# Kernel optimization log

Hardware: AMD Instinct MI355X
Metric: run time of the kernel (lower is better)

Reference implementation:

```python
import jax, jax.numpy as jnp
import numpy as np

B, S, E, H, O = 4, 2048, 1024, 8, 128

def setup_inputs() -> dict:
    key = jax.random.key(0)
    k1, k2, k3, k4, k5 = jax.random.split(key, 5)
    return {
        "x":  jax.random.normal(k1, (B, S, E), dtype=jnp.float32),
        "Wq": jax.random.normal(k2, (H, E, O), dtype=jnp.float32),
        "Wk": jax.random.normal(k3, (E, O), dtype=jnp.float32),
        "Wv": jax.random.normal(k4, (E, O), dtype=jnp.float32),
        "Wo": jax.random.normal(k5, (O * H, E), dtype=jnp.float32),
    }

def reference(x, Wq, Wk, Wv, Wo):
    # self-attention: kv = x; mode='multihead' (no causal mask), attn_mask=None
    Q = jnp.einsum('bse,heo->bhso', x, Wq)        # (B,H,S,O) per-head query proj
    K = x @ Wk                                     # (B,S,O) shared across heads
    V = x @ Wv                                     # (B,S,O)
    scale = 1.0 / jnp.sqrt(jnp.float32(O))
    scores = jnp.einsum('bhqo,bko->bhqk', Q, K) * scale  # (B,H,S,S)
    probs = jax.nn.softmax(scores, axis=-1)
    ctx = jnp.einsum('bhqk,bko->bhqo', probs, V)   # (B,H,S,O)
    ctx = ctx.transpose(0, 2, 1, 3).reshape(B, S, H * O)  # (B,S,H*O)
    return ctx @ Wo                                # (B,S,E)
```

## Files before the change

### kernel.cpp

```cpp
#include <hip/hip_runtime.h>
#include <math.h>


typedef __attribute__((ext_vector_type(8))) short bf16x8;
typedef __attribute__((ext_vector_type(4))) float f32x4;

#define MFMA(a, b, c) __builtin_amdgcn_mfma_f32_16x16x32_bf16((a), (b), (c), 0, 0, 0)
#define GLB(p) ((const __attribute__((address_space(1))) void*)(p))
#define LDS(p) ((__attribute__((address_space(3))) void*)(p))

#if __has_builtin(__builtin_amdgcn_exp2f)
#define EXP2F(x) __builtin_amdgcn_exp2f(x)
#else
#define EXP2F(x) exp2f(x)
#endif

__device__ __forceinline__ short f2bf(float f) {
    union { float f; unsigned u; } v; v.f = f;
    unsigned r = v.u + 0x7fffu + ((v.u >> 16) & 1u);
    return (short)(r >> 16);
}
__device__ __forceinline__ float bf2f(short s) {
    union { unsigned u; float f; } v; v.u = ((unsigned)(unsigned short)s) << 16;
    return v.f;
}


__global__ __launch_bounds__(256) void split_kernel(
    const float* __restrict__ x, short* __restrict__ hi, short* __restrict__ lo, int n) {
    for (int i = blockIdx.x * blockDim.x + threadIdx.x; i < n; i += gridDim.x * blockDim.x) {
        float f = x[i];
        short h = f2bf(f);
        hi[i] = h;
        lo[i] = f2bf(f - bf2f(h));
    }
}

__global__ __launch_bounds__(256) void build_wt(
    const float* __restrict__ Wq, const float* __restrict__ Wk, const float* __restrict__ Wv,
    short* __restrict__ wth, short* __restrict__ wtl) {
    const int total = 1280 * 1024;
    for (int idx = blockIdx.x * blockDim.x + threadIdx.x; idx < total; idx += gridDim.x * blockDim.x) {
        int n = idx >> 10, k = idx & 1023;
        float f;
        if (n < 1024)      f = Wq[((size_t)(n >> 7) * 1024 + k) * 128 + (n & 127)];
        else if (n < 1152) f = Wk[(size_t)k * 128 + (n - 1024)];
        else               f = Wv[(size_t)k * 128 + (n - 1152)];
        short h = f2bf(f);
        wth[idx] = h;
        wtl[idx] = f2bf(f - bf2f(h));
    }
}

__global__ __launch_bounds__(256) void build_wot(
    const float* __restrict__ Wo, short* __restrict__ wot) {
    const int total = 1024 * 1024;
    for (int idx = blockIdx.x * blockDim.x + threadIdx.x; idx < total; idx += gridDim.x * blockDim.x) {
        int e = idx >> 10, k = idx & 1023;
        wot[idx] = f2bf(Wo[(size_t)k * 1024 + e]);
    }
}

template <int MODE>
__global__ __launch_bounds__(256, 4) void gemm_k(
    const short* __restrict__ Ah, const short* __restrict__ Al,
    const short* __restrict__ Bth, const short* __restrict__ Btl,
    short* __restrict__ qh, short* __restrict__ ql,
    short* __restrict__ kh, short* __restrict__ kl,
    short* __restrict__ vt, float* __restrict__ outf) {
    constexpr int K = 1024;
    __shared__ __align__(16) char smem[33792];
    short* As_h = (short*)smem;
    short* Bs_h = (short*)(smem + 8192);
    short* As_l = (short*)(smem + 16384);
    short* Bs_l = (short*)(smem + 24576);
    unsigned* Ep = (unsigned*)smem;

    const int t = threadIdx.x;
    const int m0 = blockIdx.x * 128, n0 = blockIdx.y * 128;
    const int wave = t >> 6, lane = t & 63;
    const int wr = wave >> 1, wc = wave & 1;
    const int quad = lane >> 4, l16 = lane & 15;

    f32x4 acc[4][4];
    for (int i = 0; i < 4; ++i)
        for (int j = 0; j < 4; ++j) acc[i][j] = (f32x4){0.f, 0.f, 0.f, 0.f};

    for (int kb = 0; kb < K / 32; ++kb) {
        __syncthreads();
        for (int i = 0; i < 2; ++i) {
            int slot = (wave * 2 + i) * 64 + lane;
            int row = slot >> 2, ch = slot & 3;
            int ldsoff = (wave * 2 + i) * 512;
            size_t ga = (size_t)(m0 + row) * K + kb * 32 + ch * 8;
            size_t gb = (size_t)(n0 + row) * K + kb * 32 + ch * 8;
            __builtin_amdgcn_global_load_lds(GLB(Ah + ga), LDS(&As_h[ldsoff]), 16, 0, 0);
            __builtin_amdgcn_global_load_lds(GLB(Bth + gb), LDS(&Bs_h[ldsoff]), 16, 0, 0);
            if constexpr (MODE == 0) {
                __builtin_amdgcn_global_load_lds(GLB(Al + ga), LDS(&As_l[ldsoff]), 16, 0, 0);
                __builtin_amdgcn_global_load_lds(GLB(Btl + gb), LDS(&Bs_l[ldsoff]), 16, 0, 0);
            }
        }
        __syncthreads();

        bf16x8 a[4], b[4];
        for (int mi = 0; mi < 4; ++mi)
            a[mi] = *(const bf16x8*)&As_h[(wr * 64 + mi * 16 + l16) * 32 + quad * 8];
        for (int ni = 0; ni < 4; ++ni)
            b[ni] = *(const bf16x8*)&Bs_h[(wc * 64 + ni * 16 + l16) * 32 + quad * 8];
        for (int mi = 0; mi < 4; ++mi)
            for (int ni = 0; ni < 4; ++ni)
                acc[mi][ni] = MFMA(a[mi], b[ni], acc[mi][ni]);
        if constexpr (MODE == 0) {
            bf16x8 al[4], bl[4];
            for (int mi = 0; mi < 4; ++mi)
                al[mi] = *(const bf16x8*)&As_l[(wr * 64 + mi * 16 + l16) * 32 + quad * 8];
            for (int ni = 0; ni < 4; ++ni)
                bl[ni] = *(const bf16x8*)&Bs_l[(wc * 64 + ni * 16 + l16) * 32 + quad * 8];
            for (int mi = 0; mi < 4; ++mi)
                for (int ni = 0; ni < 4; ++ni) {
                    acc[mi][ni] = MFMA(a[mi], bl[ni], acc[mi][ni]);
                    acc[mi][ni] = MFMA(al[mi], b[ni], acc[mi][ni]);
                }
        }
    }

    const float qscale = 0.12753102455195157f;
    for (int p = 0; p < 2; ++p) {
        __syncthreads();
        if (wr == p) {
            for (int mi = 0; mi < 4; ++mi) {
                int rl = mi * 16 + quad * 4;
                for (int ni = 0; ni < 4; ++ni) {
                    int cl = wc * 64 + ni * 16 + l16;
                    for (int r = 0; r < 4; ++r) {
                        float v = acc[mi][ni][r];
                        unsigned pk;
                        if constexpr (MODE == 0) {
                            if (blockIdx.y < 8) v *= qscale;
                            short hv = f2bf(v);
                            short lv = f2bf(v - bf2f(hv));
                            pk = (unsigned)(unsigned short)hv |
                                 ((unsigned)(unsigned short)lv << 16);
                        } else {
                            union { float f; unsigned u; } cv; cv.f = v; pk = cv.u;
                        }
                        Ep[(rl + r) * 132 + cl] = pk;
                    }
                }
            }
        }
        __syncthreads();

        if constexpr (MODE == 1) {
            for (int j = 0; j < 8; ++j) {
                int cid = t + j * 256;
                int row = cid >> 5, c = cid & 31;
                f32x4 val;
                for (int q = 0; q < 4; ++q) {
                    union { unsigned u; float f; } cv;
                    cv.u = Ep[row * 132 + c * 4 + q];
                    val[q] = cv.f;
                }
                int gr = m0 + p * 64 + row;
                *(f32x4*)&outf[(size_t)gr * 1024 + n0 + c * 4] = val;
            }
        } else if (blockIdx.y < 9) {
            for (int j = 0; j < 4; ++j) {
                int cid = t + j * 256;
                int row = cid >> 4, c = cid & 15;
                bf16x8 hv, lv;
                for (int q = 0; q < 8; ++q) {
                    unsigned w = Ep[row * 132 + c * 8 + q];
                    hv[q] = (short)(w & 0xffffu);
                    lv[q] = (short)(w >> 16);
                }
                int gr = m0 + p * 64 + row;
                int bb = gr >> 11, s = gr & 2047;
                if (blockIdx.y < 8) {
                    size_t base = (((size_t)(bb * 8 + (n0 >> 7))) * 2048 + s) * 128 + c * 8;
                    *(bf16x8*)&qh[base] = hv;
                    *(bf16x8*)&ql[base] = lv;
                } else {
                    size_t base = ((size_t)bb * 2048 + s) * 128 + c * 8;
                    *(bf16x8*)&kh[base] = hv;
                    *(bf16x8*)&kl[base] = lv;
                }
            }
        } else {
            for (int j = 0; j < 4; ++j) {
                int cid = t + j * 256;
                int d = cid >> 3, sc = cid & 7;
                bf16x8 hv;
                for (int q = 0; q < 8; ++q) {
                    unsigned w = Ep[(sc * 8 + q) * 132 + d];
                    hv[q] = (short)(w & 0xffffu);
                }
                int gr0 = m0 + p * 64 + sc * 8;
                int bb = gr0 >> 11, s0 = gr0 & 2047;
                *(bf16x8*)&vt[((size_t)bb * 128 + d) * 2048 + s0] = hv;
            }
        }
    }
}

__global__ __launch_bounds__(256, 2) void attn_k(
    const short* __restrict__ qh, const short* __restrict__ ql,
    const short* __restrict__ kh, const short* __restrict__ kl,
    const short* __restrict__ vt, short* __restrict__ ctx) {
    constexpr int S = 2048, D = 128;
    __shared__ short Kh_s[64 * 128];
    __shared__ short Kl_s[64 * 128];
    __shared__ short Vt_s[128 * 64];
    __shared__ short P_s[128 * 72];

    const int bh = blockIdx.y, b = bh >> 3, h = bh & 7;
    const int q0 = blockIdx.x * 128;
    const int t = threadIdx.x, wave = t >> 6, lane = t & 63;
    const int quad = lane >> 4, l16 = lane & 15;
    const int e8 = l16 & 7;

    bf16x8 bones;
    {
        short o = (l16 == 0) ? (short)0x3F80 : (short)0;
        for (int j = 0; j < 8; ++j) bones[j] = o;
    }

    bf16x8 qfh[2][4], qfl[2][4];
    for (int mb = 0; mb < 2; ++mb) {
        size_t qbase = ((size_t)(b * 8 + h) * S + q0 + wave * 32 + mb * 16 + l16) * D + quad * 8;
        for (int c = 0; c < 4; ++c) {
            qfh[mb][c] = *(const bf16x8*)(qh + qbase + c * 32);
            qfl[mb][c] = *(const bf16x8*)(ql + qbase + c * 32);
        }
    }

    float mrow[2][4];
    f32x4 oacc[2][8], lacc[2];
    for (int mb = 0; mb < 2; ++mb) {
        for (int r = 0; r < 4; ++r) mrow[mb][r] = -INFINITY;
        for (int oi = 0; oi < 8; ++oi) oacc[mb][oi] = (f32x4){0.f, 0.f, 0.f, 0.f};
        lacc[mb] = (f32x4){0.f, 0.f, 0.f, 0.f};
    }

    for (int kt = 0; kt < S / 64; ++kt) {
        __syncthreads();
        {
            int pch = lane & 15;
            for (int i = 0; i < 4; ++i) {
                int rk = wave * 16 + i * 4 + (lane >> 4);
                int j = pch ^ (rk & 7);
                size_t g = ((size_t)b * S + kt * 64 + rk) * D + j * 8;
                int ldsoff = (wave * 16 + i * 4) * 128;
                __builtin_amdgcn_global_load_lds(GLB(kh + g), LDS(&Kh_s[ldsoff]), 16, 0, 0);
                __builtin_amdgcn_global_load_lds(GLB(kl + g), LDS(&Kl_s[ldsoff]), 16, 0, 0);
            }
        }
        {
            int pch = lane & 7;
            for (int i = 0; i < 4; ++i) {
                int rv = wave * 32 + i * 8 + (lane >> 3);
                int j = pch ^ (rv & 7);
                size_t g = ((size_t)b * D + rv) * S + kt * 64 + j * 8;
                int ldsoff = (wave * 32 + i * 8) * 64;
                __builtin_amdgcn_global_load_lds(GLB(vt + g), LDS(&Vt_s[ldsoff]), 16, 0, 0);
            }
        }
        __syncthreads();

        f32x4 sacc[2][4];
        for (int mb = 0; mb < 2; ++mb)
            for (int ni = 0; ni < 4; ++ni) sacc[mb][ni] = (f32x4){0.f, 0.f, 0.f, 0.f};
        for (int ni = 0; ni < 4; ++ni) {
            for (int c = 0; c < 4; ++c) {
                int off = (ni * 16 + l16) * 128 + ((c * 4 + quad) ^ e8) * 8;
                bf16x8 kbh = *(const bf16x8*)&Kh_s[off];
                bf16x8 kbl = *(const bf16x8*)&Kl_s[off];
                __builtin_amdgcn_s_setprio(1);
                for (int mb = 0; mb < 2; ++mb) {
                    sacc[mb][ni] = MFMA(qfh[mb][c], kbh, sacc[mb][ni]);
                    sacc[mb][ni] = MFMA(qfl[mb][c], kbh, sacc[mb][ni]);
                    sacc[mb][ni] = MFMA(qfh[mb][c], kbl, sacc[mb][ni]);
                }
                __builtin_amdgcn_s_setprio(0);
            }
        }

        for (int mb = 0; mb < 2; ++mb) {
            for (int r = 0; r < 4; ++r) {
                float mx = fmaxf(fmaxf(sacc[mb][0][r], sacc[mb][1][r]),
                                 fmaxf(sacc[mb][2][r], sacc[mb][3][r]));
                for (int off = 8; off; off >>= 1) mx = fmaxf(mx, __shfl_xor(mx, off));
                float mnew = fmaxf(mrow[mb][r], mx);
                float alpha = EXP2F(mrow[mb][r] - mnew);
                mrow[mb][r] = mnew;
                for (int ni = 0; ni < 4; ++ni)
                    sacc[mb][ni][r] = EXP2F(sacc[mb][ni][r] - mnew);
                lacc[mb][r] *= alpha;
                for (int oi = 0; oi < 8; ++oi) oacc[mb][oi][r] *= alpha;
            }
            for (int ni = 0; ni < 4; ++ni)
                for (int r = 0; r < 4; ++r) {
                    union { float f; unsigned u; } cv; cv.f = sacc[mb][ni][r];
                    P_s[(wave * 32 + mb * 16 + quad * 4 + r) * 72 + ni * 16 + l16] =
                        (short)((cv.u + 0x8000u) >> 16);
                }
        }

        for (int c2 = 0; c2 < 2; ++c2) {
            bf16x8 pa[2];
            for (int mb = 0; mb < 2; ++mb) {
                pa[mb] = *(const bf16x8*)&P_s[(wave * 32 + mb * 16 + l16) * 72 + c2 * 32 + quad * 8];
                lacc[mb] = MFMA(pa[mb], bones, lacc[mb]);
            }
            for (int oi = 0; oi < 8; ++oi) {
                int off = (oi * 16 + l16) * 64 + ((c2 * 4 + quad) ^ e8) * 8;
                bf16x8 vb = *(const bf16x8*)&Vt_s[off];
                __builtin_amdgcn_s_setprio(1);
                for (int mb = 0; mb < 2; ++mb)
                    oacc[mb][oi] = MFMA(pa[mb], vb, oacc[mb][oi]);
                __builtin_amdgcn_s_setprio(0);
            }
        }
    }

    for (int mb = 0; mb < 2; ++mb) {
        for (int r = 0; r < 4; ++r) {
            float ls = __shfl(lacc[mb][r], lane & 48);
            float inv = 1.f / ls;
            int s = q0 + wave * 32 + mb * 16 + quad * 4 + r;
            size_t base = ((size_t)b * S + s) * 1024 + h * 128;
            for (int oi = 0; oi < 8; ++oi)
                ctx[base + oi * 16 + l16] = f2bf(oacc[mb][oi][r] * inv);
        }
    }
}


extern "C" void kernel_launch(void* const* d_in, const int* in_sizes, int n_in,
                              void* d_out, int out_size, void* d_ws, size_t ws_size,
                              hipStream_t stream) {
    const float* x  = (const float*)d_in[0];
    const float* Wq = (const float*)d_in[1];
    const float* Wk = (const float*)d_in[2];
    const float* Wv = (const float*)d_in[3];
    const float* Wo = (const float*)d_in[4];
    float* out = (float*)d_out;

    char* p = (char*)d_ws;
    auto alloc = [&](size_t bytes) { char* r = p; p += bytes; return r; };
    short* xh  = (short*)alloc(16777216);
    short* xl  = (short*)alloc(16777216);
    short* wth = (short*)alloc(2621440);
    short* wtl = (short*)alloc(2621440);
    short* wot = (short*)alloc(2097152);
    short* qh  = (short*)alloc(16777216);
    short* ql  = (short*)alloc(16777216);
    short* kh  = (short*)alloc(2097152);
    short* kl  = (short*)alloc(2097152);
    short* vt  = (short*)alloc(2097152);
    short* ctx = (short*)alloc(16777216);

    split_kernel<<<dim3(2048), dim3(256), 0, stream>>>(x, xh, xl, 8192 * 1024);
    build_wt<<<dim3(1280), dim3(256), 0, stream>>>(Wq, Wk, Wv, wth, wtl);
    build_wot<<<dim3(1024), dim3(256), 0, stream>>>(Wo, wot);
    gemm_k<0><<<dim3(64, 10), dim3(256), 0, stream>>>(xh, xl, wth, wtl,
                                                      qh, ql, kh, kl, vt, nullptr);
    attn_k<<<dim3(16, 32), dim3(256), 0, stream>>>(qh, ql, kh, kl, vt, ctx);
    gemm_k<1><<<dim3(64, 8), dim3(256), 0, stream>>>(ctx, nullptr, wot, nullptr,
                                                     nullptr, nullptr, nullptr, nullptr,
                                                     nullptr, out);
}
```

Before: 359.6 us.

## Double-buffer K/V tiles in attention and enlarge blocks to 512 threads

The attention kernel now uses double-buffered LDS for the K-hi, K-lo and V tiles. The next tile's global-to-LDS loads are issued before the current tile is computed, and the two syncthreads per iteration become one waitcnt plus barrier at the end. Blocks grow to 512 threads covering 256 queries, which halves the grid to 256 workgroups, and the workgroup index is swizzled to remap it to (batch, head, query-block). This is meant to hide load latency and share each K/V tile across more query rows. In exchange LDS use roughly doubles, which may limit occupancy, and the smaller grid may fill the CUs less well.

```diff
diff --git a/kernel.cpp b/kernel.cpp
--- a/kernel.cpp
+++ b/kernel.cpp
@@ -204,21 +204,46 @@
     }
 }
 
-__global__ __launch_bounds__(256, 2) void attn_k(
+__global__ __launch_bounds__(512, 2) void attn_k(
     const short* __restrict__ qh, const short* __restrict__ ql,
     const short* __restrict__ kh, const short* __restrict__ kl,
     const short* __restrict__ vt, short* __restrict__ ctx) {
     constexpr int S = 2048, D = 128;
-    __shared__ short Kh_s[64 * 128];
-    __shared__ short Kl_s[64 * 128];
-    __shared__ short Vt_s[128 * 64];
-    __shared__ short P_s[128 * 72];
-
-    const int bh = blockIdx.y, b = bh >> 3, h = bh & 7;
-    const int q0 = blockIdx.x * 128;
+    __shared__ short Kh_s[2][64 * 128];
+    __shared__ short Kl_s[2][64 * 128];
+    __shared__ short Vt_s[2][128 * 64];
+    __shared__ short P_s[256 * 72];
+
+    const int wg = blockIdx.x;
+    const int swz = (wg & 7) * 32 + (wg >> 3);
+    const int bh = swz >> 3, b = bh >> 3, h = bh & 7;
+    const int q0 = (swz & 7) * 256;
     const int t = threadIdx.x, wave = t >> 6, lane = t & 63;
     const int quad = lane >> 4, l16 = lane & 15;
     const int e8 = l16 & 7;
+
+    auto stage = [&](int bufi, int kt) {
+        short* KhB = Kh_s[bufi];
+        short* KlB = Kl_s[bufi];
+        short* VtB = Vt_s[bufi];
+        int pch = lane & 15;
+        for (int i = 0; i < 2; ++i) {
+            int rk = wave * 8 + i * 4 + (lane >> 4);
+            int j = pch ^ (rk & 7);
+            size_t g = ((size_t)b * S + kt * 64 + rk) * D + j * 8;
+            int ldsoff = (wave * 8 + i * 4) * 128;
+            __builtin_amdgcn_global_load_lds(GLB(kh + g), LDS(&KhB[ldsoff]), 16, 0, 0);
+            __builtin_amdgcn_global_load_lds(GLB(kl + g), LDS(&KlB[ldsoff]), 16, 0, 0);
+        }
+        int pv = lane & 7;
+        for (int i = 0; i < 2; ++i) {
+            int rv = wave * 16 + i * 8 + (lane >> 3);
+            int j = pv ^ (rv & 7);
+            size_t g = ((size_t)b * D + rv) * S + kt * 64 + j * 8;
+            int ldsoff = (wave * 16 + i * 8) * 64;
+            __builtin_amdgcn_global_load_lds(GLB(vt + g), LDS(&VtB[ldsoff]), 16, 0, 0);
+        }
+    };
 
     bf16x8 bones;
     {
@@ -243,30 +268,18 @@
         lacc[mb] = (f32x4){0.f, 0.f, 0.f, 0.f};
     }
 
+    stage(0, 0);
+    asm volatile("s_waitcnt vmcnt(0)" ::: "memory");
+    __builtin_amdgcn_s_barrier();
+    __builtin_amdgcn_sched_barrier(0);
+
     for (int kt = 0; kt < S / 64; ++kt) {
-        __syncthreads();
-        {
-            int pch = lane & 15;
-            for (int i = 0; i < 4; ++i) {
-                int rk = wave * 16 + i * 4 + (lane >> 4);
-                int j = pch ^ (rk & 7);
-                size_t g = ((size_t)b * S + kt * 64 + rk) * D + j * 8;
-                int ldsoff = (wave * 16 + i * 4) * 128;
-                __builtin_amdgcn_global_load_lds(GLB(kh + g), LDS(&Kh_s[ldsoff]), 16, 0, 0);
-                __builtin_amdgcn_global_load_lds(GLB(kl + g), LDS(&Kl_s[ldsoff]), 16, 0, 0);
-            }
-        }
-        {
-            int pch = lane & 7;
-            for (int i = 0; i < 4; ++i) {
-                int rv = wave * 32 + i * 8 + (lane >> 3);
-                int j = pch ^ (rv & 7);
-                size_t g = ((size_t)b * D + rv) * S + kt * 64 + j * 8;
-                int ldsoff = (wave * 32 + i * 8) * 64;
-                __builtin_amdgcn_global_load_lds(GLB(vt + g), LDS(&Vt_s[ldsoff]), 16, 0, 0);
-            }
-        }
-        __syncthreads();
+        const int cur = kt & 1;
+        if (kt + 1 < S / 64) stage(cur ^ 1, kt + 1);
+
+        const short* KhC = Kh_s[cur];
+        const short* KlC = Kl_s[cur];
+        const short* VtC = Vt_s[cur];
 
         f32x4 sacc[2][4];
         for (int mb = 0; mb < 2; ++mb)
@@ -274,8 +287,8 @@
         for (int ni = 0; ni < 4; ++ni) {
             for (int c = 0; c < 4; ++c) {
                 int off = (ni * 16 + l16) * 128 + ((c * 4 + quad) ^ e8) * 8;
-                bf16x8 kbh = *(const bf16x8*)&Kh_s[off];
-                bf16x8 kbl = *(const bf16x8*)&Kl_s[off];
+                bf16x8 kbh = *(const bf16x8*)&KhC[off];
+                bf16x8 kbl = *(const bf16x8*)&KlC[off];
                 __builtin_amdgcn_s_setprio(1);
                 for (int mb = 0; mb < 2; ++mb) {
                     sacc[mb][ni] = MFMA(qfh[mb][c], kbh, sacc[mb][ni]);
@@ -315,13 +328,18 @@
             }
             for (int oi = 0; oi < 8; ++oi) {
                 int off = (oi * 16 + l16) * 64 + ((c2 * 4 + quad) ^ e8) * 8;
-                bf16x8 vb = *(const bf16x8*)&Vt_s[off];
+                bf16x8 vb = *(const bf16x8*)&VtC[off];
                 __builtin_amdgcn_s_setprio(1);
                 for (int mb = 0; mb < 2; ++mb)
                     oacc[mb][oi] = MFMA(pa[mb], vb, oacc[mb][oi]);
                 __builtin_amdgcn_s_setprio(0);
             }
         }
+
+        asm volatile("s_waitcnt vmcnt(0)" ::: "memory");
+        __builtin_amdgcn_sched_barrier(0);
+        __builtin_amdgcn_s_barrier();
+        __builtin_amdgcn_sched_barrier(0);
     }
 
     for (int mb = 0; mb < 2; ++mb) {
@@ -366,7 +384,7 @@
     build_wot<<<dim3(1024), dim3(256), 0, stream>>>(Wo, wot);
     gemm_k<0><<<dim3(64, 10), dim3(256), 0, stream>>>(xh, xl, wth, wtl,
                                                       qh, ql, kh, kl, vt, nullptr);
-    attn_k<<<dim3(16, 32), dim3(256), 0, stream>>>(qh, ql, kh, kl, vt, ctx);
+    attn_k<<<dim3(256), dim3(512), 0, stream>>>(qh, ql, kh, kl, vt, ctx);
     gemm_k<1><<<dim3(64, 8), dim3(256), 0, stream>>>(ctx, nullptr, wot, nullptr,
                                                      nullptr, nullptr, nullptr, nullptr,
                                                      nullptr, out);
```

New measurement: 355.3 us. No clear change (-1.2%).

## Shrink attention tiles to 64 queries and 32 keys, add lazy softmax rescale

Applied to the files above, without the earlier changes.

The attention kernel now gives each block 64 query rows (16 per wave) and walks keys in 32-wide tiles. LDS use drops and launch bounds rise to 4 blocks per CU, and the grid doubles to 1024 blocks. It also skips the online-softmax rescale unless some row max grows by more than 8, which removes exp and multiply work on most tiles. The cost is that each K/V tile is reused by half as many query rows, so global and LDS traffic per FLOP rise, and more barriers run per key. The lazy max lets exponent arguments reach up to 2^8 before rescaling.

```diff
diff --git a/kernel.cpp b/kernel.cpp
--- a/kernel.cpp
+++ b/kernel.cpp
@@ -204,21 +204,22 @@
     }
 }
 
-__global__ __launch_bounds__(256, 2) void attn_k(
+__global__ __launch_bounds__(256, 4) void attn_k(
     const short* __restrict__ qh, const short* __restrict__ ql,
     const short* __restrict__ kh, const short* __restrict__ kl,
     const short* __restrict__ vt, short* __restrict__ ctx) {
     constexpr int S = 2048, D = 128;
-    __shared__ short Kh_s[64 * 128];
-    __shared__ short Kl_s[64 * 128];
-    __shared__ short Vt_s[128 * 64];
-    __shared__ short P_s[128 * 72];
+    __shared__ short Kh_s[32 * 128];
+    __shared__ short Kl_s[32 * 128];
+    __shared__ short Vt_s[128 * 32];
+    __shared__ short P_s[64 * 40];
 
     const int bh = blockIdx.y, b = bh >> 3, h = bh & 7;
-    const int q0 = blockIdx.x * 128;
+    const int q0 = blockIdx.x * 64;
     const int t = threadIdx.x, wave = t >> 6, lane = t & 63;
     const int quad = lane >> 4, l16 = lane & 15;
     const int e8 = l16 & 7;
+    const int e4 = l16 & 3;
 
     bf16x8 bones;
     {
@@ -226,113 +227,108 @@
         for (int j = 0; j < 8; ++j) bones[j] = o;
     }
 
-    bf16x8 qfh[2][4], qfl[2][4];
-    for (int mb = 0; mb < 2; ++mb) {
-        size_t qbase = ((size_t)(b * 8 + h) * S + q0 + wave * 32 + mb * 16 + l16) * D + quad * 8;
+    bf16x8 qfh[4], qfl[4];
+    {
+        size_t qbase = ((size_t)(b * 8 + h) * S + q0 + wave * 16 + l16) * D + quad * 8;
         for (int c = 0; c < 4; ++c) {
-            qfh[mb][c] = *(const bf16x8*)(qh + qbase + c * 32);
-            qfl[mb][c] = *(const bf16x8*)(ql + qbase + c * 32);
-        }
-    }
-
-    float mrow[2][4];
-    f32x4 oacc[2][8], lacc[2];
-    for (int mb = 0; mb < 2; ++mb) {
-        for (int r = 0; r < 4; ++r) mrow[mb][r] = -INFINITY;
-        for (int oi = 0; oi < 8; ++oi) oacc[mb][oi] = (f32x4){0.f, 0.f, 0.f, 0.f};
-        lacc[mb] = (f32x4){0.f, 0.f, 0.f, 0.f};
-    }
-
-    for (int kt = 0; kt < S / 64; ++kt) {
+            qfh[c] = *(const bf16x8*)(qh + qbase + c * 32);
+            qfl[c] = *(const bf16x8*)(ql + qbase + c * 32);
+        }
+    }
+
+    float mrow[4];
+    f32x4 oacc[8], lacc;
+    for (int r = 0; r < 4; ++r) mrow[r] = -INFINITY;
+    for (int oi = 0; oi < 8; ++oi) oacc[oi] = (f32x4){0.f, 0.f, 0.f, 0.f};
+    lacc = (f32x4){0.f, 0.f, 0.f, 0.f};
+
+    for (int kt = 0; kt < S / 32; ++kt) {
         __syncthreads();
         {
             int pch = lane & 15;
-            for (int i = 0; i < 4; ++i) {
-                int rk = wave * 16 + i * 4 + (lane >> 4);
+            for (int i = 0; i < 2; ++i) {
+                int rk = wave * 8 + i * 4 + (lane >> 4);
                 int j = pch ^ (rk & 7);
-                size_t g = ((size_t)b * S + kt * 64 + rk) * D + j * 8;
-                int ldsoff = (wave * 16 + i * 4) * 128;
+                size_t g = ((size_t)b * S + kt * 32 + rk) * D + j * 8;
+                int ldsoff = (wave * 8 + i * 4) * 128;
                 __builtin_amdgcn_global_load_lds(GLB(kh + g), LDS(&Kh_s[ldsoff]), 16, 0, 0);
                 __builtin_amdgcn_global_load_lds(GLB(kl + g), LDS(&Kl_s[ldsoff]), 16, 0, 0);
             }
         }
         {
-            int pch = lane & 7;
-            for (int i = 0; i < 4; ++i) {
-                int rv = wave * 32 + i * 8 + (lane >> 3);
-                int j = pch ^ (rv & 7);
-                size_t g = ((size_t)b * D + rv) * S + kt * 64 + j * 8;
-                int ldsoff = (wave * 32 + i * 8) * 64;
+            int pv = lane & 3;
+            for (int i = 0; i < 2; ++i) {
+                int rv = wave * 32 + i * 16 + (lane >> 2);
+                int j = pv ^ (rv & 3);
+                size_t g = ((size_t)b * D + rv) * S + kt * 32 + j * 8;
+                int ldsoff = (wave * 32 + i * 16) * 32;
                 __builtin_amdgcn_global_load_lds(GLB(vt + g), LDS(&Vt_s[ldsoff]), 16, 0, 0);
             }
         }
         __syncthreads();
 
-        f32x4 sacc[2][4];
-        for (int mb = 0; mb < 2; ++mb)
-            for (int ni = 0; ni < 4; ++ni) sacc[mb][ni] = (f32x4){0.f, 0.f, 0.f, 0.f};
-        for (int ni = 0; ni < 4; ++ni) {
+        f32x4 sacc[2];
+        for (int ni = 0; ni < 2; ++ni) sacc[ni] = (f32x4){0.f, 0.f, 0.f, 0.f};
+        for (int ni = 0; ni < 2; ++ni) {
             for (int c = 0; c < 4; ++c) {
                 int off = (ni * 16 + l16) * 128 + ((c * 4 + quad) ^ e8) * 8;
                 bf16x8 kbh = *(const bf16x8*)&Kh_s[off];
                 bf16x8 kbl = *(const bf16x8*)&Kl_s[off];
                 __builtin_amdgcn_s_setprio(1);
-                for (int mb = 0; mb < 2; ++mb) {
-                    sacc[mb][ni] = MFMA(qfh[mb][c], kbh, sacc[mb][ni]);
-                    sacc[mb][ni] = MFMA(qfl[mb][c], kbh, sacc[mb][ni]);
-                    sacc[mb][ni] = MFMA(qfh[mb][c], kbl, sacc[mb][ni]);
-                }
+                sacc[ni] = MFMA(qfh[c], kbh, sacc[ni]);
+                sacc[ni] = MFMA(qfl[c], kbh, sacc[ni]);
+                sacc[ni] = MFMA(qfh[c], kbl, sacc[ni]);
                 __builtin_amdgcn_s_setprio(0);
             }
         }
 
-        for (int mb = 0; mb < 2; ++mb) {
+        float rmx[4];
+        for (int r = 0; r < 4; ++r) {
+            float mx = fmaxf(sacc[0][r], sacc[1][r]);
+            for (int off = 8; off; off >>= 1) mx = fmaxf(mx, __shfl_xor(mx, off));
+            rmx[r] = mx;
+        }
+        bool grow = false;
+        for (int r = 0; r < 4; ++r) grow |= (rmx[r] > mrow[r] + 8.0f);
+        if (__any(grow)) {
             for (int r = 0; r < 4; ++r) {
-                float mx = fmaxf(fmaxf(sacc[mb][0][r], sacc[mb][1][r]),
-                                 fmaxf(sacc[mb][2][r], sacc[mb][3][r]));
-                for (int off = 8; off; off >>= 1) mx = fmaxf(mx, __shfl_xor(mx, off));
-                float mnew = fmaxf(mrow[mb][r], mx);
-                float alpha = EXP2F(mrow[mb][r] - mnew);
-                mrow[mb][r] = mnew;
-                for (int ni = 0; ni < 4; ++ni)
-                    sacc[mb][ni][r] = EXP2F(sacc[mb][ni][r] - mnew);
-                lacc[mb][r] *= alpha;
-                for (int oi = 0; oi < 8; ++oi) oacc[mb][oi][r] *= alpha;
-            }
-            for (int ni = 0; ni < 4; ++ni)
-                for (int r = 0; r < 4; ++r) {
-                    union { float f; unsigned u; } cv; cv.f = sacc[mb][ni][r];
-                    P_s[(wave * 32 + mb * 16 + quad * 4 + r) * 72 + ni * 16 + l16] =
-                        (short)((cv.u + 0x8000u) >> 16);
-                }
-        }
-
-        for (int c2 = 0; c2 < 2; ++c2) {
-            bf16x8 pa[2];
-            for (int mb = 0; mb < 2; ++mb) {
-                pa[mb] = *(const bf16x8*)&P_s[(wave * 32 + mb * 16 + l16) * 72 + c2 * 32 + quad * 8];
-                lacc[mb] = MFMA(pa[mb], bones, lacc[mb]);
-            }
+                float mnew = fmaxf(mrow[r], rmx[r]);
+                float alpha = EXP2F(mrow[r] - mnew);
+                mrow[r] = mnew;
+                lacc[r] *= alpha;
+                for (int oi = 0; oi < 8; ++oi) oacc[oi][r] *= alpha;
+            }
+        }
+        for (int ni = 0; ni < 2; ++ni)
+            for (int r = 0; r < 4; ++r)
+                sacc[ni][r] = EXP2F(sacc[ni][r] - mrow[r]);
+        for (int ni = 0; ni < 2; ++ni)
+            for (int r = 0; r < 4; ++r) {
+                union { float f; unsigned u; } cv; cv.f = sacc[ni][r];
+                P_s[(wave * 16 + quad * 4 + r) * 40 + ni * 16 + l16] =
+                    (short)((cv.u + 0x8000u) >> 16);
+            }
+
+        {
+            bf16x8 pa = *(const bf16x8*)&P_s[(wave * 16 + l16) * 40 + quad * 8];
+            lacc = MFMA(pa, bones, lacc);
             for (int oi = 0; oi < 8; ++oi) {
-                int off = (oi * 16 + l16) * 64 + ((c2 * 4 + quad) ^ e8) * 8;
+                int off = (oi * 16 + l16) * 32 + (quad ^ e4) * 8;
                 bf16x8 vb = *(const bf16x8*)&Vt_s[off];
                 __builtin_amdgcn_s_setprio(1);
-                for (int mb = 0; mb < 2; ++mb)
-                    oacc[mb][oi] = MFMA(pa[mb], vb, oacc[mb][oi]);
+                oacc[oi] = MFMA(pa, vb, oacc[oi]);
                 __builtin_amdgcn_s_setprio(0);
             }
         }
     }
 
-    for (int mb = 0; mb < 2; ++mb) {
-        for (int r = 0; r < 4; ++r) {
-            float ls = __shfl(lacc[mb][r], lane & 48);
-            float inv = 1.f / ls;
-            int s = q0 + wave * 32 + mb * 16 + quad * 4 + r;
-            size_t base = ((size_t)b * S + s) * 1024 + h * 128;
-            for (int oi = 0; oi < 8; ++oi)
-                ctx[base + oi * 16 + l16] = f2bf(oacc[mb][oi][r] * inv);
-        }
+    for (int r = 0; r < 4; ++r) {
+        float ls = __shfl(lacc[r], lane & 48);
+        float inv = 1.f / ls;
+        int s = q0 + wave * 16 + quad * 4 + r;
+        size_t base = ((size_t)b * S + s) * 1024 + h * 128;
+        for (int oi = 0; oi < 8; ++oi)
+            ctx[base + oi * 16 + l16] = f2bf(oacc[oi][r] * inv);
     }
 }
 
@@ -366,7 +362,7 @@
     build_wot<<<dim3(1024), dim3(256), 0, stream>>>(Wo, wot);
     gemm_k<0><<<dim3(64, 10), dim3(256), 0, stream>>>(xh, xl, wth, wtl,
                                                       qh, ql, kh, kl, vt, nullptr);
-    attn_k<<<dim3(16, 32), dim3(256), 0, stream>>>(qh, ql, kh, kl, vt, ctx);
+    attn_k<<<dim3(32, 32), dim3(256), 0, stream>>>(qh, ql, kh, kl, vt, ctx);
     gemm_k<1><<<dim3(64, 8), dim3(256), 0, stream>>>(ctx, nullptr, wot, nullptr,
                                                      nullptr, nullptr, nullptr, nullptr,
                                                      nullptr, out);
```

Result: slower. 412.3 us (+14.7%).
